# Kernel optimization log

Measured on AMD Instinct MI355X. Metric: run time of the kernel, lower is better.

The kernel has to match this reference:

```python
import jax, jax.numpy as jnp
import numpy as np

B, S, D = 4, 2048, 1024
H = 16
HD = D // H  # head_dim = 64


def setup_inputs() -> dict:
    key = jax.random.key(0)
    ks = jax.random.split(key, 8)
    scale = 1.0 / np.sqrt(D)
    return {
        "X_Q": jax.random.normal(ks[0], (B, S, D), dtype=jnp.float32),
        "X_KV": jax.random.normal(ks[1], (B, S, D), dtype=jnp.float32),
        # q_proj: Linear(D, D), weights stored as (in, out)
        "q_w": jax.random.normal(ks[2], (D, D), dtype=jnp.float32) * scale,
        "q_b": jax.random.normal(ks[3], (D,), dtype=jnp.float32) * scale,
        # kv_proj: Linear(D, 2*D)
        "kv_w": jax.random.normal(ks[4], (D, 2 * D), dtype=jnp.float32) * scale,
        "kv_b": jax.random.normal(ks[5], (2 * D,), dtype=jnp.float32) * scale,
        # out_proj: Linear(D, D) (query_dim == input_dim)
        "out_w": jax.random.normal(ks[6], (D, D), dtype=jnp.float32) * scale,
        "out_b": jax.random.normal(ks[7], (D,), dtype=jnp.float32) * scale,
    }


def reference(X_Q, X_KV, q_w, q_b, kv_w, kv_b, out_w, out_b):
    # projections
    q = X_Q @ q_w + q_b                      # [b, s, D]
    kv = X_KV @ kv_w + kv_b                  # [b, l, 2D]
    k, v = jnp.split(kv, 2, axis=-1)         # each [b, l, D]

    def split_heads(t):
        b, m, _ = t.shape
        return t.reshape(b, m, H, HD).transpose(0, 2, 1, 3)  # [b, h, m, d]

    q, k, v = split_heads(q), split_heads(k), split_heads(v)

    # standard attention: full SxL scores (non-flash path)
    scores = jnp.einsum("bhsd,bhld->bhsl", q, k) / np.sqrt(HD)
    attn = jax.nn.softmax(scores, axis=-1)   # dropout_p = 0 -> identity
    out = jnp.einsum("bhsl,bhld->bhsd", attn, v)

    # merge heads: [b, h, s, d] -> [b, s, h*d]
    out = out.transpose(0, 2, 1, 3).reshape(B, S, D)
    return out @ out_w + out_b
```

## Files before the change

### kernel.cpp

```cpp
#include <hip/hip_runtime.h>
#include <hip/hip_bf16.h>
#include <math.h>

#define B_  4
#define S_  2048
#define D_  1024
#define H_  16
#define HD_ 64

typedef __bf16 bf16;
typedef __bf16 bf16x4 __attribute__((ext_vector_type(4)));
typedef __bf16 bf16x8 __attribute__((ext_vector_type(8)));
typedef float  floatx4 __attribute__((ext_vector_type(4)));

#define QSCALE 0.18033688011112042f

__device__ __forceinline__ void async_load16(const bf16* g, bf16* l) {
  __builtin_amdgcn_global_load_lds(
      (const __attribute__((address_space(1))) void*)g,
      (__attribute__((address_space(3))) void*)l, 16, 0, 0);
}

__global__ __launch_bounds__(256) void cast_both(
    const float* __restrict__ ina, bf16* __restrict__ outa,
    const float* __restrict__ inb, bf16* __restrict__ outb) {
  int bid = blockIdx.x;
  const float* in;
  bf16* out;
  int i;
  if (bid < 8192) { in = ina; out = outa; i = (bid * 256 + threadIdx.x) * 4; }
  else            { in = inb; out = outb; i = ((bid - 8192) * 256 + threadIdx.x) * 4; }
  float4 v = *reinterpret_cast<const float4*>(in + i);
  bf16x4 o;
  o[0] = (bf16)v.x; o[1] = (bf16)v.y; o[2] = (bf16)v.z; o[3] = (bf16)v.w;
  *reinterpret_cast<bf16x4*>(out + i) = o;
}

__global__ __launch_bounds__(256) void transcast_all(
    const float* __restrict__ qw, bf16* __restrict__ qwT,
    const float* __restrict__ kvw, bf16* __restrict__ kvwT,
    const float* __restrict__ ow, bf16* __restrict__ owT) {
  __shared__ float tile[32][33];
  int bid = blockIdx.x;
  const float* in; bf16* out; int N, lb;
  if (bid < 1024)      { in = qw;  out = qwT;  N = 1024; lb = bid; }
  else if (bid < 3072) { in = kvw; out = kvwT; N = 2048; lb = bid - 1024; }
  else                 { in = ow;  out = owT;  N = 1024; lb = bid - 3072; }
  int nx = N >> 5;
  int n0 = (lb % nx) * 32, k0 = (lb / nx) * 32;
  int tx = threadIdx.x & 31, ty = threadIdx.x >> 5;
  #pragma unroll
  for (int i = ty; i < 32; i += 8)
    tile[i][tx] = in[(size_t)(k0 + i) * N + n0 + tx];
  __syncthreads();
  #pragma unroll
  for (int i = ty; i < 32; i += 8)
    out[(size_t)(n0 + i) * 1024 + k0 + tx] = (bf16)tile[tx][i];
}

template <int MODE>
__device__ __forceinline__ void gemm_body(
    const bf16* __restrict__ A, const bf16* __restrict__ Bt,
    const float* __restrict__ bias, void* __restrict__ out,
    int M, int N, int K, int bx, int by,
    bf16 (*As)[64], bf16 (*Bs)[64]) {
  const int tid  = threadIdx.x;
  const int m0   = by * 128;
  const int n0   = bx * 128;
  const int w    = tid >> 6;
  const int lane = tid & 63;
  const int lr   = lane & 15;
  const int lq   = lane >> 4;
  const int wm   = (w >> 1) * 64;
  const int wn   = (w & 1) * 64;

  const int srow = lane >> 3;
  const int sg   = (lane & 7) ^ srow;
  const bf16* aptr = A  + (size_t)(m0 + 32 * w + srow) * K + 8 * sg;
  const bf16* bptr = Bt + (size_t)(n0 + 32 * w + srow) * K + 8 * sg;

  floatx4 acc[4][4];
  #pragma unroll
  for (int i = 0; i < 4; i++)
    #pragma unroll
    for (int j = 0; j < 4; j++)
      acc[i][j] = floatx4{0.f, 0.f, 0.f, 0.f};

  for (int k0 = 0; k0 < K; k0 += 64) {
    __syncthreads();
    #pragma unroll
    for (int p = 0; p < 4; p++) {
      async_load16(aptr + (size_t)8 * p * K + k0, &As[32 * w + 8 * p][0]);
      async_load16(bptr + (size_t)8 * p * K + k0, &Bs[32 * w + 8 * p][0]);
    }
    __syncthreads();
    #pragma unroll
    for (int kc = 0; kc < 2; kc++) {
      const int sw = 8 * ((kc * 4 + lq) ^ (lr & 7));
      bf16x8 af[4], bfv[4];
      #pragma unroll
      for (int t = 0; t < 4; t++)
        af[t] = *reinterpret_cast<const bf16x8*>(&As[wm + 16 * t + lr][sw]);
      #pragma unroll
      for (int t = 0; t < 4; t++)
        bfv[t] = *reinterpret_cast<const bf16x8*>(&Bs[wn + 16 * t + lr][sw]);
      #pragma unroll
      for (int i = 0; i < 4; i++)
        #pragma unroll
        for (int j = 0; j < 4; j++)
          acc[i][j] = __builtin_amdgcn_mfma_f32_16x16x32_bf16(af[i], bfv[j], acc[i][j], 0, 0, 0);
    }
  }

  #pragma unroll
  for (int i = 0; i < 4; i++) {
    int row_base = m0 + wm + 16 * i + lq * 4;
    #pragma unroll
    for (int j = 0; j < 4; j++) {
      int col = n0 + wn + 16 * j + lr;
      float bv = bias[col];
      if (MODE == 2 && col >= 1024) {
        int b = row_base >> 11, s0 = row_base & 2047;
        int c = col - 1024, h = c >> 6, d = c & 63;
        bf16* Vt = (bf16*)out + (size_t)B_ * H_ * S_ * HD_;
        bf16x4 pk;
        #pragma unroll
        for (int r = 0; r < 4; r++) pk[r] = (bf16)(acc[i][j][r] + bv);
        *reinterpret_cast<bf16x4*>(
            &Vt[(((size_t)b * H_ + h) * HD_ + d) * S_ + s0]) = pk;
        continue;
      }
      #pragma unroll
      for (int r = 0; r < 4; r++) {
        int row = row_base + r;
        float v = acc[i][j][r] + bv;
        if (MODE == 0) {
          ((float*)out)[(size_t)row * N + col] = v;
        } else if (MODE == 1) {
          int b = row >> 11, s = row & 2047;
          int h = col >> 6, d = col & 63;
          ((bf16*)out)[(((size_t)b * H_ + h) * S_ + s) * HD_ + d] =
              (bf16)(v * QSCALE);
        } else {
          int b = row >> 11, s = row & 2047;
          int h = col >> 6, d = col & 63;
          ((bf16*)out)[(((size_t)b * H_ + h) * S_ + s) * HD_ + d] = (bf16)v;
        }
      }
    }
  }
}

__global__ __launch_bounds__(256) void gemm_out(
    const bf16* __restrict__ A, const bf16* __restrict__ Bt,
    const float* __restrict__ bias, void* __restrict__ out,
    int M, int N, int K) {
  __shared__ bf16 As[128][64];
  __shared__ bf16 Bs[128][64];
  gemm_body<0>(A, Bt, bias, out, M, N, K, blockIdx.x, blockIdx.y, As, Bs);
}

__global__ __launch_bounds__(256) void gemm_qkv(
    const bf16* __restrict__ Xq, const bf16* __restrict__ qwT,
    const float* __restrict__ q_b, bf16* __restrict__ Qb,
    const bf16* __restrict__ Xkv, const bf16* __restrict__ kvwT,
    const float* __restrict__ kv_b, bf16* __restrict__ KVb) {
  __shared__ bf16 As[128][64];
  __shared__ bf16 Bs[128][64];
  int bid = blockIdx.x;
  if (bid < 512) {
    gemm_body<1>(Xq, qwT, q_b, Qb, 8192, 1024, 1024, bid & 7, bid >> 3, As, Bs);
  } else {
    int b2 = bid - 512;
    gemm_body<2>(Xkv, kvwT, kv_b, KVb, 8192, 2048, 1024, b2 & 15, b2 >> 4, As, Bs);
  }
}

__global__ __launch_bounds__(256, 2) void attn_kernel(
    const bf16* __restrict__ Q, const bf16* __restrict__ Kb,
    const bf16* __restrict__ Vt, bf16* __restrict__ out) {
  __shared__ bf16 smem[32768];

  const int tid  = threadIdx.x;
  const int w    = tid >> 6;
  const int lane = tid & 63;
  const int lr   = lane & 15;
  const int lq   = lane >> 4;
  const int bh   = blockIdx.x;
  const int q0   = blockIdx.y * 256;
  const size_t base = (size_t)bh * S_ * HD_;

  bf16* pw = smem + 16384 + w * 4096;

  const int srow = lane >> 3;
  const int sg   = (lane & 7) ^ srow;

  const bf16* kptr = Kb + base + (size_t)(16 * w + srow) * HD_ + 8 * sg;
  const bf16* vptr = Vt + base + (size_t)(16 * w + srow) * S_  + 8 * sg;

  #pragma unroll
  for (int p = 0; p < 2; p++) {
    async_load16(kptr + (size_t)8 * p * HD_, smem + (16 * w + 8 * p) * 64);
    async_load16(vptr + (size_t)8 * p * S_,  smem + 4096 + (16 * w + 8 * p) * 64);
  }

  bf16x8 bq[4][2];
  #pragma unroll
  for (int g = 0; g < 4; g++) {
    const bf16* qrow = Q + base + (size_t)(q0 + 64 * w + 16 * g + lr) * HD_;
    bq[g][0] = *reinterpret_cast<const bf16x8*>(qrow + lq * 8);
    bq[g][1] = *reinterpret_cast<const bf16x8*>(qrow + 32 + lq * 8);
  }

  const int sw0 = 8 * ((0 + lq) ^ (lr & 7));
  const int sw1 = 8 * ((4 + lq) ^ (lr & 7));
  const int pcolbase = 4 * (lq & 1);
  const int pswz = lr & 7;

  float l_i[4] = {0.f, 0.f, 0.f, 0.f};
  floatx4 o_acc[4][4];
  #pragma unroll
  for (int g = 0; g < 4; g++)
    #pragma unroll
    for (int t = 0; t < 4; t++) o_acc[g][t] = floatx4{0.f, 0.f, 0.f, 0.f};

  __syncthreads();

  const bf16* kpf = kptr + (size_t)64 * HD_;
  const bf16* vpf = vptr + 64;

  const int NIT = S_ / 64;
  for (int it = 0; it < NIT; it++) {
    bf16* ks  = smem + (it & 1) * 8192;
    bf16* vts = ks + 4096;

    if (it + 1 < NIT) {
      bf16* ksn = smem + ((it + 1) & 1) * 8192;
      #pragma unroll
      for (int p = 0; p < 2; p++) {
        async_load16(kpf + (size_t)8 * p * HD_, ksn + (16 * w + 8 * p) * 64);
        async_load16(vpf + (size_t)8 * p * S_,  ksn + 4096 + (16 * w + 8 * p) * 64);
      }
    }

    auto qkt = [&](int t) {
      bf16x8 ak0 = *reinterpret_cast<const bf16x8*>(ks + (16 * t + lr) * 64 + sw0);
      bf16x8 ak1 = *reinterpret_cast<const bf16x8*>(ks + (16 * t + lr) * 64 + sw1);
      floatx4 sc[4];
      #pragma unroll
      for (int g = 0; g < 4; g++) {
        sc[g] = __builtin_amdgcn_mfma_f32_16x16x32_bf16(ak0, bq[g][0],
                    floatx4{0.f, 0.f, 0.f, 0.f}, 0, 0, 0);
        sc[g] = __builtin_amdgcn_mfma_f32_16x16x32_bf16(ak1, bq[g][1], sc[g], 0, 0, 0);
      }
      const int pcol = 8 * ((2 * t + (lq >> 1)) ^ pswz) + pcolbase;
      #pragma unroll
      for (int g = 0; g < 4; g++) {
        bf16x4 pk;
        float lsum = 0.f;
        #pragma unroll
        for (int r = 0; r < 4; r++) {
          float p = __builtin_amdgcn_exp2f(sc[g][r]);
          lsum += p;
          pk[r] = (bf16)p;
        }
        l_i[g] += lsum;
        *reinterpret_cast<bf16x4*>(&pw[(16 * g + lr) * 64 + pcol]) = pk;
      }
    };

    qkt(0);
    qkt(1);
    __builtin_amdgcn_wave_barrier();

    {
      bf16x8 bp0[4], av0[4];
      #pragma unroll
      for (int g = 0; g < 4; g++)
        bp0[g] = *reinterpret_cast<const bf16x8*>(&pw[(16 * g + lr) * 64 + sw0]);
      #pragma unroll
      for (int t2 = 0; t2 < 4; t2++)
        av0[t2] = *reinterpret_cast<const bf16x8*>(vts + (16 * t2 + lr) * 64 + sw0);
      qkt(2);
      __builtin_amdgcn_s_setprio(1);
      #pragma unroll
      for (int t2 = 0; t2 < 2; t2++)
        #pragma unroll
        for (int g = 0; g < 4; g++)
          o_acc[g][t2] = __builtin_amdgcn_mfma_f32_16x16x32_bf16(av0[t2], bp0[g], o_acc[g][t2], 0, 0, 0);
      __builtin_amdgcn_s_setprio(0);
      qkt(3);
      __builtin_amdgcn_s_setprio(1);
      #pragma unroll
      for (int t2 = 2; t2 < 4; t2++)
        #pragma unroll
        for (int g = 0; g < 4; g++)
          o_acc[g][t2] = __builtin_amdgcn_mfma_f32_16x16x32_bf16(av0[t2], bp0[g], o_acc[g][t2], 0, 0, 0);
      __builtin_amdgcn_s_setprio(0);
    }
    __builtin_amdgcn_wave_barrier();

    {
      bf16x8 bp1[4];
      #pragma unroll
      for (int g = 0; g < 4; g++)
        bp1[g] = *reinterpret_cast<const bf16x8*>(&pw[(16 * g + lr) * 64 + sw1]);
      __builtin_amdgcn_s_setprio(1);
      #pragma unroll
      for (int t2 = 0; t2 < 4; t2++) {
        bf16x8 av = *reinterpret_cast<const bf16x8*>(vts + (16 * t2 + lr) * 64 + sw1);
        #pragma unroll
        for (int g = 0; g < 4; g++)
          o_acc[g][t2] = __builtin_amdgcn_mfma_f32_16x16x32_bf16(av, bp1[g], o_acc[g][t2], 0, 0, 0);
      }
      __builtin_amdgcn_s_setprio(0);
    }

    kpf += (size_t)64 * HD_;
    vpf += 64;
    __syncthreads();
  }

  #pragma unroll
  for (int g = 0; g < 4; g++) {
    l_i[g] += __shfl_xor(l_i[g], 16, 64);
    l_i[g] += __shfl_xor(l_i[g], 32, 64);
  }

  const int b = bh >> 4, h = bh & 15;
  #pragma unroll
  for (int g = 0; g < 4; g++) {
    const float inv = 1.0f / l_i[g];
    const int qrow = q0 + 64 * w + 16 * g + lr;
    bf16* orow = out + ((size_t)b * S_ + qrow) * D_ + h * HD_;
    #pragma unroll
    for (int t = 0; t < 4; t++) {
      bf16x4 pk;
      #pragma unroll
      for (int r = 0; r < 4; r++) pk[r] = (bf16)(o_acc[g][t][r] * inv);
      *reinterpret_cast<bf16x4*>(&orow[16 * t + lq * 4]) = pk;
    }
  }
}

extern "C" void kernel_launch(void* const* d_in, const int* in_sizes, int n_in,
                              void* d_out, int out_size, void* d_ws, size_t ws_size,
                              hipStream_t stream) {
  const float* X_Q   = (const float*)d_in[0];
  const float* X_KV  = (const float*)d_in[1];
  const float* q_w   = (const float*)d_in[2];
  const float* q_b   = (const float*)d_in[3];
  const float* kv_w  = (const float*)d_in[4];
  const float* kv_b  = (const float*)d_in[5];
  const float* out_w = (const float*)d_in[6];
  const float* out_b = (const float*)d_in[7];
  float* out = (float*)d_out;

  char* ws = (char*)d_ws;
  const size_t MB = 1024 * 1024;
  bf16* Xq   = (bf16*)(ws + 0);
  bf16* Xkv  = (bf16*)(ws + 16 * MB);
  bf16* Qb   = (bf16*)(ws + 32 * MB);
  bf16* Kb   = (bf16*)(ws + 48 * MB);
  bf16* qwT  = (bf16*)(ws + 80 * MB);
  bf16* kvwT = (bf16*)(ws + 82 * MB);
  bf16* owT  = (bf16*)(ws + 86 * MB);
  bf16* Vt   = Kb + (size_t)B_ * H_ * S_ * HD_;
  bf16* attn = Xq;

  cast_both<<<16384, 256, 0, stream>>>(X_Q, Xq, X_KV, Xkv);
  transcast_all<<<4096, 256, 0, stream>>>(q_w, qwT, kv_w, kvwT, out_w, owT);

  gemm_qkv<<<1536, 256, 0, stream>>>(Xq, qwT, q_b, Qb, Xkv, kvwT, kv_b, Kb);
  attn_kernel<<<dim3(64, 8), 256, 0, stream>>>(Qb, Kb, Vt, attn);
  gemm_out<<<dim3(8, 64), 256, 0, stream>>>(attn, owT, out_b, out, 8192, 1024, 1024);
}
```

Baseline: 309.0 us.

## Widen attention blocks to 8 waves sharing K/V tiles, halve P scratch

The attention kernel now runs 512-thread blocks covering 512 query rows each, so every K/V tile staged in LDS is reused by twice as many waves and each wave issues half as many async loads. To fit in the same LDS, each wave's P scratch is cut to 32 columns and reused between the two halves of the 64-key tile, with a new swizzle and an explicit lgkmcnt wait before it is overwritten. The grid is halved to 256 blocks, which lowers parallelism and may leave some compute units underused. The extra wait also serialises part of the P-buffer reuse.

```diff
diff --git a/kernel.cpp b/kernel.cpp
--- a/kernel.cpp
+++ b/kernel.cpp
@@ -176,7 +176,7 @@
   }
 }
 
-__global__ __launch_bounds__(256, 2) void attn_kernel(
+__global__ __launch_bounds__(512, 4) void attn_kernel(
     const bf16* __restrict__ Q, const bf16* __restrict__ Kb,
     const bf16* __restrict__ Vt, bf16* __restrict__ out) {
   __shared__ bf16 smem[32768];
@@ -187,22 +187,19 @@
   const int lr   = lane & 15;
   const int lq   = lane >> 4;
   const int bh   = blockIdx.x;
-  const int q0   = blockIdx.y * 256;
+  const int q0   = blockIdx.y * 512;
   const size_t base = (size_t)bh * S_ * HD_;
 
-  bf16* pw = smem + 16384 + w * 4096;
+  bf16* pw = smem + 16384 + w * 2048;
 
   const int srow = lane >> 3;
   const int sg   = (lane & 7) ^ srow;
 
-  const bf16* kptr = Kb + base + (size_t)(16 * w + srow) * HD_ + 8 * sg;
-  const bf16* vptr = Vt + base + (size_t)(16 * w + srow) * S_  + 8 * sg;
-
-  #pragma unroll
-  for (int p = 0; p < 2; p++) {
-    async_load16(kptr + (size_t)8 * p * HD_, smem + (16 * w + 8 * p) * 64);
-    async_load16(vptr + (size_t)8 * p * S_,  smem + 4096 + (16 * w + 8 * p) * 64);
-  }
+  const bf16* kptr = Kb + base + (size_t)(8 * w + srow) * HD_ + 8 * sg;
+  const bf16* vptr = Vt + base + (size_t)(8 * w + srow) * S_  + 8 * sg;
+
+  async_load16(kptr, smem + 8 * w * 64);
+  async_load16(vptr, smem + 4096 + 8 * w * 64);
 
   bf16x8 bq[4][2];
   #pragma unroll
@@ -214,8 +211,9 @@
 
   const int sw0 = 8 * ((0 + lq) ^ (lr & 7));
   const int sw1 = 8 * ((4 + lq) ^ (lr & 7));
+  const int pxr = lr & 3;
   const int pcolbase = 4 * (lq & 1);
-  const int pswz = lr & 7;
+  const int prd = 8 * (lq ^ pxr);
 
   float l_i[4] = {0.f, 0.f, 0.f, 0.f};
   floatx4 o_acc[4][4];
@@ -236,11 +234,8 @@
 
     if (it + 1 < NIT) {
       bf16* ksn = smem + ((it + 1) & 1) * 8192;
-      #pragma unroll
-      for (int p = 0; p < 2; p++) {
-        async_load16(kpf + (size_t)8 * p * HD_, ksn + (16 * w + 8 * p) * 64);
-        async_load16(vpf + (size_t)8 * p * S_,  ksn + 4096 + (16 * w + 8 * p) * 64);
-      }
+      async_load16(kpf, ksn + 8 * w * 64);
+      async_load16(vpf, ksn + 4096 + 8 * w * 64);
     }
 
     auto qkt = [&](int t) {
@@ -253,7 +248,7 @@
                     floatx4{0.f, 0.f, 0.f, 0.f}, 0, 0, 0);
         sc[g] = __builtin_amdgcn_mfma_f32_16x16x32_bf16(ak1, bq[g][1], sc[g], 0, 0, 0);
       }
-      const int pcol = 8 * ((2 * t + (lq >> 1)) ^ pswz) + pcolbase;
+      const int pcol = 8 * ((2 * (t & 1) + (lq >> 1)) ^ pxr) + pcolbase;
       #pragma unroll
       for (int g = 0; g < 4; g++) {
         bf16x4 pk;
@@ -265,7 +260,7 @@
           pk[r] = (bf16)p;
         }
         l_i[g] += lsum;
-        *reinterpret_cast<bf16x4*>(&pw[(16 * g + lr) * 64 + pcol]) = pk;
+        *reinterpret_cast<bf16x4*>(&pw[(16 * g + lr) * 32 + pcol]) = pk;
       }
     };
 
@@ -273,38 +268,40 @@
     qkt(1);
     __builtin_amdgcn_wave_barrier();
 
-    {
-      bf16x8 bp0[4], av0[4];
+    bf16x8 bp0[4];
+    #pragma unroll
+    for (int g = 0; g < 4; g++)
+      bp0[g] = *reinterpret_cast<const bf16x8*>(&pw[(16 * g + lr) * 32 + prd]);
+    asm volatile("s_waitcnt lgkmcnt(0)" ::: "memory");
+    __builtin_amdgcn_wave_barrier();
+
+    qkt(2);
+    __builtin_amdgcn_s_setprio(1);
+    #pragma unroll
+    for (int t2 = 0; t2 < 2; t2++) {
+      bf16x8 av = *reinterpret_cast<const bf16x8*>(vts + (16 * t2 + lr) * 64 + sw0);
       #pragma unroll
       for (int g = 0; g < 4; g++)
-        bp0[g] = *reinterpret_cast<const bf16x8*>(&pw[(16 * g + lr) * 64 + sw0]);
-      #pragma unroll
-      for (int t2 = 0; t2 < 4; t2++)
-        av0[t2] = *reinterpret_cast<const bf16x8*>(vts + (16 * t2 + lr) * 64 + sw0);
-      qkt(2);
-      __builtin_amdgcn_s_setprio(1);
-      #pragma unroll
-      for (int t2 = 0; t2 < 2; t2++)
-        #pragma unroll
-        for (int g = 0; g < 4; g++)
-          o_acc[g][t2] = __builtin_amdgcn_mfma_f32_16x16x32_bf16(av0[t2], bp0[g], o_acc[g][t2], 0, 0, 0);
-      __builtin_amdgcn_s_setprio(0);
-      qkt(3);
-      __builtin_amdgcn_s_setprio(1);
-      #pragma unroll
-      for (int t2 = 2; t2 < 4; t2++)
-        #pragma unroll
-        for (int g = 0; g < 4; g++)
-          o_acc[g][t2] = __builtin_amdgcn_mfma_f32_16x16x32_bf16(av0[t2], bp0[g], o_acc[g][t2], 0, 0, 0);
-      __builtin_amdgcn_s_setprio(0);
-    }
+        o_acc[g][t2] = __builtin_amdgcn_mfma_f32_16x16x32_bf16(av, bp0[g], o_acc[g][t2], 0, 0, 0);
+    }
+    __builtin_amdgcn_s_setprio(0);
+    qkt(3);
+    __builtin_amdgcn_s_setprio(1);
+    #pragma unroll
+    for (int t2 = 2; t2 < 4; t2++) {
+      bf16x8 av = *reinterpret_cast<const bf16x8*>(vts + (16 * t2 + lr) * 64 + sw0);
+      #pragma unroll
+      for (int g = 0; g < 4; g++)
+        o_acc[g][t2] = __builtin_amdgcn_mfma_f32_16x16x32_bf16(av, bp0[g], o_acc[g][t2], 0, 0, 0);
+    }
+    __builtin_amdgcn_s_setprio(0);
     __builtin_amdgcn_wave_barrier();
 
     {
       bf16x8 bp1[4];
       #pragma unroll
       for (int g = 0; g < 4; g++)
-        bp1[g] = *reinterpret_cast<const bf16x8*>(&pw[(16 * g + lr) * 64 + sw1]);
+        bp1[g] = *reinterpret_cast<const bf16x8*>(&pw[(16 * g + lr) * 32 + prd]);
       __builtin_amdgcn_s_setprio(1);
       #pragma unroll
       for (int t2 = 0; t2 < 4; t2++) {
@@ -372,6 +369,6 @@
   transcast_all<<<4096, 256, 0, stream>>>(q_w, qwT, kv_w, kvwT, out_w, owT);
 
   gemm_qkv<<<1536, 256, 0, stream>>>(Xq, qwT, q_b, Qb, Xkv, kvwT, kv_b, Kb);
-  attn_kernel<<<dim3(64, 8), 256, 0, stream>>>(Qb, Kb, Vt, attn);
+  attn_kernel<<<dim3(64, 4), 512, 0, stream>>>(Qb, Kb, Vt, attn);
   gemm_out<<<dim3(8, 64), 256, 0, stream>>>(attn, owT, out_b, out, 8192, 1024, 1024);
 }
```

Result: slower. 470.9 us (+52.4%).

## Use 256x256 double-buffered GEMM tiles with 8 waves and merge prep kernels

Applied to the files above, without the earlier changes.

Rewrites the projection GEMMs to use 256x256 output tiles per 512-thread block. K-tiles are double-buffered in LDS through async global-to-LDS loads, and MFMA sections are wrapped in s_setprio. It also merges the cast and transpose-cast kernels into one launch. Larger tiles and prefetching aim to raise data reuse and hide load latency, but far fewer blocks (384 and 128) may underfill a 256-CU GPU and leave a tail wave.

```diff
diff --git a/kernel.cpp b/kernel.cpp
--- a/kernel.cpp
+++ b/kernel.cpp
@@ -21,27 +21,25 @@
       (__attribute__((address_space(3))) void*)l, 16, 0, 0);
 }
 
-__global__ __launch_bounds__(256) void cast_both(
-    const float* __restrict__ ina, bf16* __restrict__ outa,
-    const float* __restrict__ inb, bf16* __restrict__ outb) {
-  int bid = blockIdx.x;
-  const float* in;
-  bf16* out;
-  int i;
-  if (bid < 8192) { in = ina; out = outa; i = (bid * 256 + threadIdx.x) * 4; }
-  else            { in = inb; out = outb; i = ((bid - 8192) * 256 + threadIdx.x) * 4; }
-  float4 v = *reinterpret_cast<const float4*>(in + i);
-  bf16x4 o;
-  o[0] = (bf16)v.x; o[1] = (bf16)v.y; o[2] = (bf16)v.z; o[3] = (bf16)v.w;
-  *reinterpret_cast<bf16x4*>(out + i) = o;
-}
-
-__global__ __launch_bounds__(256) void transcast_all(
+__global__ __launch_bounds__(256) void prep_all(
+    const float* __restrict__ xa, bf16* __restrict__ oa,
+    const float* __restrict__ xb, bf16* __restrict__ ob,
     const float* __restrict__ qw, bf16* __restrict__ qwT,
     const float* __restrict__ kvw, bf16* __restrict__ kvwT,
     const float* __restrict__ ow, bf16* __restrict__ owT) {
   __shared__ float tile[32][33];
   int bid = blockIdx.x;
+  if (bid < 16384) {
+    const float* in; bf16* out; int i;
+    if (bid < 8192) { in = xa; out = oa; i = (bid * 256 + threadIdx.x) * 4; }
+    else            { in = xb; out = ob; i = ((bid - 8192) * 256 + threadIdx.x) * 4; }
+    float4 v = *reinterpret_cast<const float4*>(in + i);
+    bf16x4 o;
+    o[0] = (bf16)v.x; o[1] = (bf16)v.y; o[2] = (bf16)v.z; o[3] = (bf16)v.w;
+    *reinterpret_cast<bf16x4*>(out + i) = o;
+    return;
+  }
+  bid -= 16384;
   const float* in; bf16* out; int N, lb;
   if (bid < 1024)      { in = qw;  out = qwT;  N = 1024; lb = bid; }
   else if (bid < 3072) { in = kvw; out = kvwT; N = 2048; lb = bid - 1024; }
@@ -58,66 +56,130 @@
     out[(size_t)(n0 + i) * 1024 + k0 + tx] = (bf16)tile[tx][i];
 }
 
+__device__ __forceinline__ void stage256(
+    const bf16* aptr, const bf16* bptr, int K, bf16* sbase, int kb, int k0) {
+  bf16* la = sbase + kb * 16384;
+  bf16* lb = sbase + 32768 + kb * 16384;
+  #pragma unroll
+  for (int h = 0; h < 2; h++)
+    #pragma unroll
+    for (int p = 0; p < 2; p++) {
+      const size_t off = (size_t)(h * 128 + p * 64) * K + k0;
+      async_load16(aptr + off, la + h * 8192 + p * 4096);
+      async_load16(bptr + off, lb + h * 8192 + p * 4096);
+    }
+}
+
 template <int MODE>
-__device__ __forceinline__ void gemm_body(
+__device__ __forceinline__ void gemm256_body(
     const bf16* __restrict__ A, const bf16* __restrict__ Bt,
     const float* __restrict__ bias, void* __restrict__ out,
-    int M, int N, int K, int bx, int by,
-    bf16 (*As)[64], bf16 (*Bs)[64]) {
+    int N, int K, int bx, int by, bf16* lds) {
   const int tid  = threadIdx.x;
-  const int m0   = by * 128;
-  const int n0   = bx * 128;
   const int w    = tid >> 6;
   const int lane = tid & 63;
   const int lr   = lane & 15;
   const int lq   = lane >> 4;
-  const int wm   = (w >> 1) * 64;
-  const int wn   = (w & 1) * 64;
-
+  const int wm2  = w >> 2;
+  const int wn4  = w & 3;
+  const int m0   = by * 256;
+  const int n0   = bx * 256;
   const int srow = lane >> 3;
   const int sg   = (lane & 7) ^ srow;
-  const bf16* aptr = A  + (size_t)(m0 + 32 * w + srow) * K + 8 * sg;
-  const bf16* bptr = Bt + (size_t)(n0 + 32 * w + srow) * K + 8 * sg;
-
-  floatx4 acc[4][4];
-  #pragma unroll
-  for (int i = 0; i < 4; i++)
+
+  const bf16* aptr = A  + (size_t)(m0 + w * 8 + srow) * K + 8 * sg;
+  const bf16* bptr = Bt + (size_t)(n0 + w * 8 + srow) * K + 8 * sg;
+  bf16* sbase = lds + w * 512;
+
+  const int sw0 = 8 * (lq ^ (lr & 7));
+  const int sw1 = 8 * ((4 + lq) ^ (lr & 7));
+  const bf16* aB = lds + wm2 * 8192 + lr * 64;
+  const bf16* bB = lds + 32768 + (wn4 >> 1) * 8192 + ((wn4 & 1) * 64 + lr) * 64;
+
+  floatx4 acc[8][4];
+  #pragma unroll
+  for (int i = 0; i < 8; i++)
+    #pragma unroll
+    for (int j = 0; j < 4; j++) acc[i][j] = floatx4{0.f, 0.f, 0.f, 0.f};
+
+  stage256(aptr, bptr, K, sbase, 0, 0);
+  stage256(aptr, bptr, K, sbase, 1, 64);
+  asm volatile("s_waitcnt vmcnt(8)" ::: "memory");
+  __syncthreads();
+
+  const int NK = K >> 6;
+  for (int kt = 0; kt < NK; kt++) {
+    const int kb = kt & 1;
+    const bf16* ab = aB + kb * 16384;
+    const bf16* bb = bB + kb * 16384;
+    bf16x8 af[4], bfv[4];
+
     #pragma unroll
     for (int j = 0; j < 4; j++)
-      acc[i][j] = floatx4{0.f, 0.f, 0.f, 0.f};
-
-  for (int k0 = 0; k0 < K; k0 += 64) {
+      bfv[j] = *reinterpret_cast<const bf16x8*>(bb + j * 1024 + sw0);
+    #pragma unroll
+    for (int i = 0; i < 4; i++)
+      af[i] = *reinterpret_cast<const bf16x8*>(ab + i * 1024 + sw0);
+    __builtin_amdgcn_s_setprio(1);
+    #pragma unroll
+    for (int i = 0; i < 4; i++)
+      #pragma unroll
+      for (int j = 0; j < 4; j++)
+        acc[i][j] = __builtin_amdgcn_mfma_f32_16x16x32_bf16(af[i], bfv[j], acc[i][j], 0, 0, 0);
+    __builtin_amdgcn_s_setprio(0);
+
+    #pragma unroll
+    for (int i = 0; i < 4; i++)
+      af[i] = *reinterpret_cast<const bf16x8*>(ab + (4 + i) * 1024 + sw0);
+    __builtin_amdgcn_s_setprio(1);
+    #pragma unroll
+    for (int i = 0; i < 4; i++)
+      #pragma unroll
+      for (int j = 0; j < 4; j++)
+        acc[4 + i][j] = __builtin_amdgcn_mfma_f32_16x16x32_bf16(af[i], bfv[j], acc[4 + i][j], 0, 0, 0);
+    __builtin_amdgcn_s_setprio(0);
+
+    #pragma unroll
+    for (int j = 0; j < 4; j++)
+      bfv[j] = *reinterpret_cast<const bf16x8*>(bb + j * 1024 + sw1);
+    #pragma unroll
+    for (int i = 0; i < 4; i++)
+      af[i] = *reinterpret_cast<const bf16x8*>(ab + i * 1024 + sw1);
+    __builtin_amdgcn_s_setprio(1);
+    #pragma unroll
+    for (int i = 0; i < 4; i++)
+      #pragma unroll
+      for (int j = 0; j < 4; j++)
+        acc[i][j] = __builtin_amdgcn_mfma_f32_16x16x32_bf16(af[i], bfv[j], acc[i][j], 0, 0, 0);
+    __builtin_amdgcn_s_setprio(0);
+
+    #pragma unroll
+    for (int i = 0; i < 4; i++)
+      af[i] = *reinterpret_cast<const bf16x8*>(ab + (4 + i) * 1024 + sw1);
+    __builtin_amdgcn_s_setprio(1);
+    #pragma unroll
+    for (int i = 0; i < 4; i++)
+      #pragma unroll
+      for (int j = 0; j < 4; j++)
+        acc[4 + i][j] = __builtin_amdgcn_mfma_f32_16x16x32_bf16(af[i], bfv[j], acc[4 + i][j], 0, 0, 0);
+    __builtin_amdgcn_s_setprio(0);
+
     __syncthreads();
-    #pragma unroll
-    for (int p = 0; p < 4; p++) {
-      async_load16(aptr + (size_t)8 * p * K + k0, &As[32 * w + 8 * p][0]);
-      async_load16(bptr + (size_t)8 * p * K + k0, &Bs[32 * w + 8 * p][0]);
+    if (kt + 2 < NK) {
+      stage256(aptr, bptr, K, sbase, kb, (kt + 2) * 64);
+      asm volatile("s_waitcnt vmcnt(8)" ::: "memory");
+    } else {
+      asm volatile("s_waitcnt vmcnt(0)" ::: "memory");
     }
     __syncthreads();
-    #pragma unroll
-    for (int kc = 0; kc < 2; kc++) {
-      const int sw = 8 * ((kc * 4 + lq) ^ (lr & 7));
-      bf16x8 af[4], bfv[4];
-      #pragma unroll
-      for (int t = 0; t < 4; t++)
-        af[t] = *reinterpret_cast<const bf16x8*>(&As[wm + 16 * t + lr][sw]);
-      #pragma unroll
-      for (int t = 0; t < 4; t++)
-        bfv[t] = *reinterpret_cast<const bf16x8*>(&Bs[wn + 16 * t + lr][sw]);
-      #pragma unroll
-      for (int i = 0; i < 4; i++)
-        #pragma unroll
-        for (int j = 0; j < 4; j++)
-          acc[i][j] = __builtin_amdgcn_mfma_f32_16x16x32_bf16(af[i], bfv[j], acc[i][j], 0, 0, 0);
-    }
-  }
-
-  #pragma unroll
-  for (int i = 0; i < 4; i++) {
-    int row_base = m0 + wm + 16 * i + lq * 4;
+  }
+
+  #pragma unroll
+  for (int i = 0; i < 8; i++) {
+    int row_base = m0 + wm2 * 128 + 16 * i + lq * 4;
     #pragma unroll
     for (int j = 0; j < 4; j++) {
-      int col = n0 + wn + 16 * j + lr;
+      int col = n0 + wn4 * 64 + 16 * j + lr;
       float bv = bias[col];
       if (MODE == 2 && col >= 1024) {
         int b = row_base >> 11, s0 = row_base & 2047;
@@ -151,29 +213,26 @@
   }
 }
 
-__global__ __launch_bounds__(256) void gemm_out(
-    const bf16* __restrict__ A, const bf16* __restrict__ Bt,
-    const float* __restrict__ bias, void* __restrict__ out,
-    int M, int N, int K) {
-  __shared__ bf16 As[128][64];
-  __shared__ bf16 Bs[128][64];
-  gemm_body<0>(A, Bt, bias, out, M, N, K, blockIdx.x, blockIdx.y, As, Bs);
-}
-
-__global__ __launch_bounds__(256) void gemm_qkv(
+__global__ __launch_bounds__(512, 1) void gemm_qkv(
     const bf16* __restrict__ Xq, const bf16* __restrict__ qwT,
     const float* __restrict__ q_b, bf16* __restrict__ Qb,
     const bf16* __restrict__ Xkv, const bf16* __restrict__ kvwT,
     const float* __restrict__ kv_b, bf16* __restrict__ KVb) {
-  __shared__ bf16 As[128][64];
-  __shared__ bf16 Bs[128][64];
+  __shared__ bf16 lds[65536];
   int bid = blockIdx.x;
-  if (bid < 512) {
-    gemm_body<1>(Xq, qwT, q_b, Qb, 8192, 1024, 1024, bid & 7, bid >> 3, As, Bs);
-  } else {
-    int b2 = bid - 512;
-    gemm_body<2>(Xkv, kvwT, kv_b, KVb, 8192, 2048, 1024, b2 & 15, b2 >> 4, As, Bs);
-  }
+  if (bid < 128)
+    gemm256_body<1>(Xq, qwT, q_b, Qb, 1024, 1024, bid & 3, bid >> 2, lds);
+  else {
+    int b2 = bid - 128;
+    gemm256_body<2>(Xkv, kvwT, kv_b, KVb, 2048, 1024, b2 & 7, b2 >> 3, lds);
+  }
+}
+
+__global__ __launch_bounds__(512, 1) void gemm_out(
+    const bf16* __restrict__ A, const bf16* __restrict__ Bt,
+    const float* __restrict__ bias, float* __restrict__ out) {
+  __shared__ bf16 lds[65536];
+  gemm256_body<0>(A, Bt, bias, out, 1024, 1024, blockIdx.x & 3, blockIdx.x >> 2, lds);
 }
 
 __global__ __launch_bounds__(256, 2) void attn_kernel(
@@ -368,10 +427,9 @@
   bf16* Vt   = Kb + (size_t)B_ * H_ * S_ * HD_;
   bf16* attn = Xq;
 
-  cast_both<<<16384, 256, 0, stream>>>(X_Q, Xq, X_KV, Xkv);
-  transcast_all<<<4096, 256, 0, stream>>>(q_w, qwT, kv_w, kvwT, out_w, owT);
-
-  gemm_qkv<<<1536, 256, 0, stream>>>(Xq, qwT, q_b, Qb, Xkv, kvwT, kv_b, Kb);
+  prep_all<<<20480, 256, 0, stream>>>(X_Q, Xq, X_KV, Xkv,
+                                      q_w, qwT, kv_w, kvwT, out_w, owT);
+  gemm_qkv<<<384, 512, 0, stream>>>(Xq, qwT, q_b, Qb, Xkv, kvwT, kv_b, Kb);
   attn_kernel<<<dim3(64, 8), 256, 0, stream>>>(Qb, Kb, Vt, attn);
-  gemm_out<<<dim3(8, 64), 256, 0, stream>>>(attn, owT, out_b, out, 8192, 1024, 1024);
-}
+  gemm_out<<<128, 512, 0, stream>>>(attn, owT, out_b, out);
+}
```

New measurement: 330.3 us. 1.07x slower.
